# Performance work log

Measured on AMD Instinct MI355X. Metric: run time of the kernel, lower is better.

## Reference

```python
import jax, jax.numpy as jnp
import numpy as np
import math

D_MODEL = 2048
NUM_HEADS = 16
HEAD_DIM = D_MODEL // NUM_HEADS  # 128
B, S = 2, 2048


def setup_inputs() -> dict:
    key = jax.random.key(0)
    ks = jax.random.split(key, 11)
    s_in = 1.0 / math.sqrt(D_MODEL)
    return {
        "query": jax.random.normal(ks[0], (B, S, D_MODEL), dtype=jnp.float32),
        "key": jax.random.normal(ks[1], (B, S, D_MODEL), dtype=jnp.float32),
        "value": jax.random.normal(ks[2], (B, S, D_MODEL), dtype=jnp.float32),
        "Wq": jax.random.normal(ks[3], (D_MODEL, D_MODEL), dtype=jnp.float32) * s_in,
        "bq": jnp.zeros((D_MODEL,), dtype=jnp.float32),
        "Wk": jax.random.normal(ks[4], (D_MODEL, HEAD_DIM), dtype=jnp.float32) * s_in,
        "bk": jnp.zeros((HEAD_DIM,), dtype=jnp.float32),
        "Wv": jax.random.normal(ks[5], (D_MODEL, HEAD_DIM), dtype=jnp.float32) * s_in,
        "bv": jnp.zeros((HEAD_DIM,), dtype=jnp.float32),
        "Wo": jax.random.normal(ks[6], (D_MODEL, D_MODEL), dtype=jnp.float32) * s_in,
        "bo": jnp.zeros((D_MODEL,), dtype=jnp.float32),
    }


def reference(query, key, value, Wq, bq, Wk, bk, Wv, bv, Wo, bo):
    b, s, d_model = query.shape
    h, d = NUM_HEADS, HEAD_DIM
    # Projections: Q has h heads, K/V have a single shared head (MQA)
    Q = (query @ Wq + bq).reshape(b, s, h, d).transpose(0, 2, 1, 3)  # [b,h,s,d]
    K = key @ Wk + bk      # [b,s,d]
    V = value @ Wv + bv    # [b,s,d]
    scale = 1.0 / math.sqrt(d)
    # broadcast single K head over all h query heads
    scores = jnp.einsum('bhqd,bkd->bhqk', Q, K) * scale  # [b,h,s,s]
    weights = jax.nn.softmax(scores, axis=-1)
    attn = jnp.einsum('bhqk,bkd->bhqd', weights, V)      # [b,h,s,d]
    attn = attn.transpose(0, 2, 1, 3).reshape(b, s, d_model)
    return attn @ Wo + bo
```

## Files before the change

### kernel.cpp

```cpp
#include <hip/hip_runtime.h>


typedef unsigned short u16;
typedef __attribute__((ext_vector_type(8))) short bf16x8;
typedef __attribute__((ext_vector_type(4))) short bf16x4;
typedef __attribute__((ext_vector_type(4))) float f32x4;

#define D_MODEL 2048
#define SEQ     2048
#define NH      16
#define HD      128
#define BK      32

__device__ __forceinline__ u16 f2bf(float f){
  union { float f; unsigned u; } v; v.f = f;
  unsigned r = (v.u + 0x7FFFu + ((v.u >> 16) & 1u)) >> 16;
  return (u16)r;
}

#if __has_builtin(__builtin_amdgcn_cvt_pk_bf16_f32)
__device__ __forceinline__ unsigned pack2bf(float a, float b){
  auto v = __builtin_amdgcn_cvt_pk_bf16_f32(a, b);
  unsigned u; __builtin_memcpy(&u, &v, 4); return u;
}
#else
__device__ __forceinline__ unsigned pack2bf(float a, float b){
  return (unsigned)f2bf(a) | ((unsigned)f2bf(b) << 16);
}
#endif

__device__ __forceinline__ void gll16(const void* g, void* l){
  __builtin_amdgcn_global_load_lds(
      (const __attribute__((address_space(1))) void*)g,
      (__attribute__((address_space(3))) void*)l, 16, 0, 0);
}

__global__ __launch_bounds__(256) void convert3_kernel(
    const float4* __restrict__ a, const float4* __restrict__ b, const float4* __restrict__ c,
    ushort4* __restrict__ oa, ushort4* __restrict__ ob, ushort4* __restrict__ oc){
  int i = blockIdx.x*256 + threadIdx.x;
  float4 va = a[i], vb = b[i], vc = c[i];
  ushort4 ra, rb, rc;
  ra.x=f2bf(va.x); ra.y=f2bf(va.y); ra.z=f2bf(va.z); ra.w=f2bf(va.w);
  rb.x=f2bf(vb.x); rb.y=f2bf(vb.y); rb.z=f2bf(vb.z); rb.w=f2bf(vb.w);
  rc.x=f2bf(vc.x); rc.y=f2bf(vc.y); rc.z=f2bf(vc.z); rc.w=f2bf(vc.w);
  oa[i]=ra; ob[i]=rb; oc[i]=rc;
}

__global__ __launch_bounds__(256) void transpose_all(
    const float* __restrict__ Wq, const float* __restrict__ Wo,
    const float* __restrict__ Wk, const float* __restrict__ Wv,
    u16* __restrict__ WqT, u16* __restrict__ WoT,
    u16* __restrict__ WkT, u16* __restrict__ WvT){
  __shared__ float tt[32][33];
  int id = blockIdx.x;
  const float* in; u16* outp; int C, bx, by;
  if (id < 4096)      { in=Wq; outp=WqT; C=2048; bx=id&63;        by=id>>6; }
  else if (id < 8192) { id-=4096; in=Wo; outp=WoT; C=2048; bx=id&63; by=id>>6; }
  else if (id < 8448) { id-=8192; in=Wk; outp=WkT; C=128;  bx=id&3;  by=id>>2; }
  else                { id-=8448; in=Wv; outp=WvT; C=128;  bx=id&3;  by=id>>2; }
  const int R = 2048;
  int c0 = bx*32, r0 = by*32;
  int tx = threadIdx.x & 31, ty = threadIdx.x >> 5;
  #pragma unroll
  for (int k=0;k<4;k++) tt[ty+k*8][tx] = in[(size_t)(r0+ty+k*8)*C + c0+tx];
  __syncthreads();
  #pragma unroll
  for (int k=0;k<4;k++) outp[(size_t)(c0+ty+k*8)*R + r0+tx] = f2bf(tt[tx][ty+k*8]);
}

__device__ __forceinline__ void gemm_core_db(
    const u16* __restrict__ A, const u16* __restrict__ BT,
    int lda, int ldb, int m0, int n0, int kbeg, int kend,
    u16* As, u16* Bs, f32x4 acc[4][4])
{
  const int t = threadIdx.x;
  const int w = t >> 6, l = t & 63;
  const int wr = w >> 1, wc = w & 1;
  const int c16 = l & 15, q = l >> 4;
  const int srow = l >> 2;
  const int sc   = ((l & 3) ^ ((l >> 3) & 3)) * 8;

  int aoff[4], boff[4];
  #pragma unroll
  for (int mt=0;mt<4;mt++){
    int row = wr*64 + mt*16 + c16;
    aoff[mt] = row*BK + ((q ^ ((row>>1)&3))*8);
  }
  #pragma unroll
  for (int nt=0;nt<4;nt++){
    int row = wc*64 + nt*16 + c16;
    boff[nt] = row*BK + ((q ^ ((row>>1)&3))*8);
  }

  auto issue = [&](int k0, int buf){
    u16* Ad = As + buf*4096;
    u16* Bd = Bs + buf*4096;
    #pragma unroll
    for (int half=0; half<2; half++){
      int r = half*64 + w*16 + srow;
      gll16(A  + (size_t)(m0+r)*lda + k0 + sc, Ad + (half*64 + w*16)*BK);
      gll16(BT + (size_t)(n0+r)*ldb + k0 + sc, Bd + (half*64 + w*16)*BK);
    }
  };

  const int n = (kend - kbeg) / BK;
  issue(kbeg, 0);
  for (int i = 0; i < n; i++){
    __syncthreads();
    if (i+1 < n) issue(kbeg + (i+1)*BK, (i+1)&1);
    const u16* Ab = As + (i&1)*4096;
    const u16* Bb = Bs + (i&1)*4096;
    bf16x8 af[4], bfr[4];
    #pragma unroll
    for (int mt=0;mt<4;mt++) af[mt]  = *(const bf16x8*)(Ab + aoff[mt]);
    #pragma unroll
    for (int nt=0;nt<4;nt++) bfr[nt] = *(const bf16x8*)(Bb + boff[nt]);
    #pragma unroll
    for (int mt=0;mt<4;mt++)
      #pragma unroll
      for (int nt=0;nt<4;nt++)
        acc[mt][nt] = __builtin_amdgcn_mfma_f32_16x16x32_bf16(af[mt], bfr[nt], acc[mt][nt], 0,0,0);
  }
}

__global__ __launch_bounds__(256) void proj_kernel(
    const u16* __restrict__ qb, const u16* __restrict__ kb, const u16* __restrict__ vb,
    const u16* __restrict__ WqT, const u16* __restrict__ WkT, const u16* __restrict__ WvT,
    const float* __restrict__ bq, u16* __restrict__ Qp, float* __restrict__ part)
{
  __shared__ u16 As[2*4096], Bs[2*4096];
  f32x4 acc[4][4];
  f32x4 z = {0.f,0.f,0.f,0.f};
  #pragma unroll
  for (int i=0;i<4;i++) for (int j=0;j<4;j++) acc[i][j] = z;
  const int t = threadIdx.x, w = t>>6, l = t&63, wr = w>>1, wc = w&1, c16 = l&15, q = l>>4;
  int id = blockIdx.x;
  if (id < 512){
    int m0 = (id & 31)*128, n0 = (id >> 5)*128;
    gemm_core_db(qb, WqT, 2048, 2048, m0, n0, 0, 2048, As, Bs, acc);
    #pragma unroll
    for (int mt=0;mt<4;mt++)
      #pragma unroll
      for (int nt=0;nt<4;nt++){
        int col = n0 + wc*64 + nt*16 + c16;
        float bv = bq[col];
        #pragma unroll
        for (int r=0;r<4;r++){
          int row = m0 + wr*64 + mt*16 + q*4 + r;
          Qp[(size_t)row*D_MODEL + col] = f2bf(acc[mt][nt][r] + bv);
        }
      }
  } else {
    int kvid = id - 512;
    int zi = kvid & 3, nb = (kvid >> 2) & 1, mi = kvid >> 3;
    const u16* Am = nb ? vb  : kb;
    const u16* Bm = nb ? WvT : WkT;
    gemm_core_db(Am, Bm, 2048, 2048, mi*128, 0, zi*512, zi*512+512, As, Bs, acc);
    float* dst = part + (size_t)(zi*2 + nb)*524288;
    #pragma unroll
    for (int mt=0;mt<4;mt++)
      #pragma unroll
      for (int nt=0;nt<4;nt++){
        int col = wc*64 + nt*16 + c16;
        #pragma unroll
        for (int r=0;r<4;r++){
          int row = mi*128 + wr*64 + mt*16 + q*4 + r;
          dst[(size_t)row*128 + col] = acc[mt][nt][r];
        }
      }
  }
}

__global__ __launch_bounds__(256) void oproj_kernel(
    const u16* __restrict__ A, const u16* __restrict__ BT, const float* __restrict__ bias,
    float* __restrict__ C)
{
  __shared__ u16 As[2*4096], Bs[2*4096];
  f32x4 acc[4][4];
  f32x4 z = {0.f,0.f,0.f,0.f};
  #pragma unroll
  for (int i=0;i<4;i++) for (int j=0;j<4;j++) acc[i][j] = z;
  int m0 = blockIdx.x*128, n0 = blockIdx.y*128;
  gemm_core_db(A, BT, 2048, 2048, m0, n0, 0, 2048, As, Bs, acc);
  const int t = threadIdx.x, w = t>>6, l = t&63, wr = w>>1, wc = w&1, c16 = l&15, q = l>>4;
  #pragma unroll
  for (int mt=0;mt<4;mt++)
    #pragma unroll
    for (int nt=0;nt<4;nt++){
      int col = n0 + wc*64 + nt*16 + c16;
      float bv = bias[col];
      #pragma unroll
      for (int r=0;r<4;r++){
        int row = m0 + wr*64 + mt*16 + q*4 + r;
        C[(size_t)row*D_MODEL + col] = acc[mt][nt][r] + bv;
      }
    }
}

__global__ __launch_bounds__(256) void kv_reduce_kernel(
    const float* __restrict__ part, const float* __restrict__ bk, const float* __restrict__ bv,
    u16* __restrict__ Kp, u16* __restrict__ VpT){
  int idx = blockIdx.x*256 + threadIdx.x;
  int d = idx & 127, sg = idx >> 7;
  float ka = 0.f, va = 0.f;
  #pragma unroll
  for (int zi=0; zi<4; zi++){
    ka += part[(size_t)(zi*2+0)*524288 + idx];
    va += part[(size_t)(zi*2+1)*524288 + idx];
  }
  Kp[idx] = f2bf(ka + bk[d]);
  int b = sg >> 11, sl = sg & 2047;
  VpT[(size_t)b*262144 + (size_t)d*2048 + sl] = f2bf(va + bv[d]);
}

__global__ __launch_bounds__(512, 2) void attn_kernel(
    const u16* __restrict__ Qp, const u16* __restrict__ Kp,
    const u16* __restrict__ VpT, u16* __restrict__ attnb){
  __shared__ u16 lds[32768];
  u16* Ks = lds;
  u16* Vs = lds + 16384;
  const int t = threadIdx.x;
  const int w = t >> 6, l = t & 63;
  const int c16 = l & 15, q = l >> 4;

  const int qt = blockIdx.x;
  const int bh = blockIdx.y;
  const int b = bh >> 4, h = bh & 15;

  const u16* Qbase = Qp  + ((size_t)(b*SEQ + qt*256 + w*32))*D_MODEL + h*HD;
  const u16* Kbase = Kp  + (size_t)(b*SEQ)*HD;
  const u16* Vbase = VpT + (size_t)b*HD*SEQ;

  #pragma unroll
  for (int j=0;j<4;j++){
    int r = j*32 + w*4 + (l >> 4);
    int g = (l & 15) ^ (r & 15);
    gll16(Kbase + (size_t)r*HD + g*8, Ks + j*4096 + w*512);
  }
  bf16x8 qf[2][4];
  #pragma unroll
  for (int qs=0;qs<2;qs++)
    #pragma unroll
    for (int kk=0;kk<4;kk++)
      qf[qs][kk] = *(const bf16x8*)(Qbase + (size_t)(qs*16 + c16)*D_MODEL + (kk*4 + q)*8);
  __syncthreads();

  f32x4 o[2][8];
  f32x4 z4 = {0.f,0.f,0.f,0.f};
  #pragma unroll
  for (int qs=0;qs<2;qs++) for (int dt=0;dt<8;dt++) o[qs][dt] = z4;
  float mrow[2] = {-1e30f, -1e30f};
  float lrow[2] = {0.f, 0.f};
  const float cs = 0.08838834764831845f * 1.4426950408889634f;

  for (int kt = 0; kt < 16; kt++){
    #pragma unroll
    for (int j=0;j<4;j++){
      int d = j*32 + w*4 + (l >> 4);
      int g = (l & 15) ^ (d & 15);
      gll16(Vbase + (size_t)d*SEQ + kt*128 + g*8, Vs + j*4096 + w*512);
    }

    f32x4 s[2][8];
    #pragma unroll
    for (int qs=0;qs<2;qs++) for (int kt8=0;kt8<8;kt8++) s[qs][kt8] = z4;
    __builtin_amdgcn_s_setprio(1);
    #pragma unroll
    for (int kt8=0; kt8<8; kt8++){
      #pragma unroll
      for (int kk=0;kk<4;kk++){
        int ch = kk*4 + q;
        bf16x8 kf = *(const bf16x8*)(Ks + (kt8*16 + c16)*128 + ((ch ^ c16) & 15)*8);
        s[0][kt8] = __builtin_amdgcn_mfma_f32_16x16x32_bf16(kf, qf[0][kk], s[0][kt8], 0,0,0);
        s[1][kt8] = __builtin_amdgcn_mfma_f32_16x16x32_bf16(kf, qf[1][kk], s[1][kt8], 0,0,0);
      }
    }
    __builtin_amdgcn_s_setprio(0);

    float alpha[2];
    #pragma unroll
    for (int qs=0; qs<2; qs++){
      float x[8];
      #pragma unroll
      for (int kt8=0;kt8<8;kt8++)
        x[kt8] = fmaxf(fmaxf(s[qs][kt8][0],s[qs][kt8][1]), fmaxf(s[qs][kt8][2],s[qs][kt8][3]));
      float vmax = fmaxf(fmaxf(fmaxf(x[0],x[1]),fmaxf(x[2],x[3])),
                         fmaxf(fmaxf(x[4],x[5]),fmaxf(x[6],x[7])));
      vmax = fmaxf(vmax, __shfl_xor(vmax, 16));
      vmax = fmaxf(vmax, __shfl_xor(vmax, 32));
      float mnew = fmaxf(mrow[qs], vmax);
      alpha[qs] = exp2f((mrow[qs] - mnew)*cs);
      float mc = mnew*cs;
      float rs[8];
      #pragma unroll
      for (int kt8=0;kt8<8;kt8++){
        float p0 = exp2f(__builtin_fmaf(s[qs][kt8][0], cs, -mc));
        float p1 = exp2f(__builtin_fmaf(s[qs][kt8][1], cs, -mc));
        float p2 = exp2f(__builtin_fmaf(s[qs][kt8][2], cs, -mc));
        float p3 = exp2f(__builtin_fmaf(s[qs][kt8][3], cs, -mc));
        s[qs][kt8][0]=p0; s[qs][kt8][1]=p1; s[qs][kt8][2]=p2; s[qs][kt8][3]=p3;
        rs[kt8] = (p0+p1)+(p2+p3);
      }
      float rsum = ((rs[0]+rs[1])+(rs[2]+rs[3])) + ((rs[4]+rs[5])+(rs[6]+rs[7]));
      rsum += __shfl_xor(rsum, 16);
      rsum += __shfl_xor(rsum, 32);
      lrow[qs] = lrow[qs]*alpha[qs] + rsum;
      mrow[qs] = mnew;
    }

    unsigned long long allone = __ballot(alpha[0] == 1.f && alpha[1] == 1.f);
    if (allone != ~0ull){
      #pragma unroll
      for (int qs=0;qs<2;qs++)
        #pragma unroll
        for (int dt=0;dt<8;dt++)
          #pragma unroll
          for (int r=0;r<4;r++) o[qs][dt][r] *= alpha[qs];
    }

    union PU { unsigned u[4]; bf16x8 v; } P32[2][4];
    #pragma unroll
    for (int qs=0;qs<2;qs++)
      #pragma unroll
      for (int kb=0;kb<4;kb++){
        P32[qs][kb].u[0] = pack2bf(s[qs][2*kb][0],   s[qs][2*kb][1]);
        P32[qs][kb].u[1] = pack2bf(s[qs][2*kb][2],   s[qs][2*kb][3]);
        P32[qs][kb].u[2] = pack2bf(s[qs][2*kb+1][0], s[qs][2*kb+1][1]);
        P32[qs][kb].u[3] = pack2bf(s[qs][2*kb+1][2], s[qs][2*kb+1][3]);
      }

    __syncthreads();

    if (kt < 15){
      #pragma unroll
      for (int j=0;j<4;j++){
        int r = j*32 + w*4 + (l >> 4);
        int g = (l & 15) ^ (r & 15);
        gll16(Kbase + (size_t)((kt+1)*128 + r)*HD + g*8, Ks + j*4096 + w*512);
      }
    }

    __builtin_amdgcn_s_setprio(1);
    #pragma unroll
    for (int kb=0; kb<4; kb++){
      int ca = 4*kb + (q>>1);
      int cb = ca + 2;
      #pragma unroll
      for (int dt=0; dt<8; dt++){
        int d = dt*16 + c16;
        union VU { bf16x4 h[2]; bf16x8 v; } vf;
        vf.h[0] = *(const bf16x4*)(Vs + d*128 + ((ca ^ c16) & 15)*8 + (q&1)*4);
        vf.h[1] = *(const bf16x4*)(Vs + d*128 + ((cb ^ c16) & 15)*8 + (q&1)*4);
        o[0][dt] = __builtin_amdgcn_mfma_f32_16x16x32_bf16(vf.v, P32[0][kb].v, o[0][dt], 0,0,0);
        o[1][dt] = __builtin_amdgcn_mfma_f32_16x16x32_bf16(vf.v, P32[1][kb].v, o[1][dt], 0,0,0);
      }
    }
    __builtin_amdgcn_s_setprio(0);
    __syncthreads();
  }

  #pragma unroll
  for (int qs=0;qs<2;qs++){
    float inv = 1.f / lrow[qs];
    int qrow = qt*256 + w*32 + qs*16 + c16;
    u16* dst = attnb + ((size_t)(b*SEQ) + qrow)*D_MODEL + h*HD + q*4;
    #pragma unroll
    for (int dt=0;dt<8;dt++){
      ushort4 pk;
      pk.x = f2bf(o[qs][dt][0]*inv);
      pk.y = f2bf(o[qs][dt][1]*inv);
      pk.z = f2bf(o[qs][dt][2]*inv);
      pk.w = f2bf(o[qs][dt][3]*inv);
      *(ushort4*)(dst + dt*16) = pk;
    }
  }
}

extern "C" void kernel_launch(void* const* d_in, const int* in_sizes, int n_in,
                              void* d_out, int out_size, void* d_ws, size_t ws_size,
                              hipStream_t stream) {
  (void)in_sizes; (void)n_in; (void)out_size; (void)ws_size;
  const float* query = (const float*)d_in[0];
  const float* key   = (const float*)d_in[1];
  const float* value = (const float*)d_in[2];
  const float* Wq    = (const float*)d_in[3];
  const float* bq    = (const float*)d_in[4];
  const float* Wk    = (const float*)d_in[5];
  const float* bk    = (const float*)d_in[6];
  const float* Wv    = (const float*)d_in[7];
  const float* bv    = (const float*)d_in[8];
  const float* Wo    = (const float*)d_in[9];
  const float* bo    = (const float*)d_in[10];
  float* out = (float*)d_out;

  char* W = (char*)d_ws;
  u16*  qb     = (u16*) (W + 0);
  u16*  kb     = (u16*) (W + 16777216);
  u16*  vb     = (u16*) (W + 33554432);
  u16*  WqT    = (u16*) (W + 50331648);
  u16*  WoT    = (u16*) (W + 58720256);
  u16*  WkT    = (u16*) (W + 67108864);
  u16*  WvT    = (u16*) (W + 67633152);
  u16*  Qp     = (u16*) (W + 68157440);
  u16*  Kp     = (u16*) (W + 84934656);
  u16*  VpT    = (u16*) (W + 85983232);
  u16*  attnb  = (u16*) (W + 87031808);
  float* kvpart= (float*)(W + 103809024);

  convert3_kernel<<<8192, 256, 0, stream>>>(
      (const float4*)query, (const float4*)key, (const float4*)value,
      (ushort4*)qb, (ushort4*)kb, (ushort4*)vb);
  transpose_all<<<8704, 256, 0, stream>>>(Wq, Wo, Wk, Wv, WqT, WoT, WkT, WvT);
  proj_kernel<<<768, 256, 0, stream>>>(qb, kb, vb, WqT, WkT, WvT, bq, Qp, kvpart);
  kv_reduce_kernel<<<2048, 256, 0, stream>>>(kvpart, bk, bv, Kp, VpT);
  attn_kernel<<<dim3(8,32), 512, 0, stream>>>(Qp, Kp, VpT, attnb);
  oproj_kernel<<<dim3(32,16), 256, 0, stream>>>(attnb, WoT, bo, out);
}
```

Measured before the change: 410.6 us.

## Double-buffer K/V tiles in attention with smaller blocks and lazy rescaling

```diff
diff --git a/kernel.cpp b/kernel.cpp
--- a/kernel.cpp
+++ b/kernel.cpp
@@ -214,12 +214,10 @@
   VpT[(size_t)b*262144 + (size_t)d*2048 + sl] = f2bf(va + bv[d]);
 }
 
-__global__ __launch_bounds__(512, 2) void attn_kernel(
+__global__ __launch_bounds__(256, 2) void attn_kernel(
     const u16* __restrict__ Qp, const u16* __restrict__ Kp,
     const u16* __restrict__ VpT, u16* __restrict__ attnb){
   __shared__ u16 lds[32768];
-  u16* Ks = lds;
-  u16* Vs = lds + 16384;
   const int t = threadIdx.x;
   const int w = t >> 6, l = t & 63;
   const int c16 = l & 15, q = l >> 4;
@@ -228,15 +226,24 @@
   const int bh = blockIdx.y;
   const int b = bh >> 4, h = bh & 15;
 
-  const u16* Qbase = Qp  + ((size_t)(b*SEQ + qt*256 + w*32))*D_MODEL + h*HD;
+  const u16* Qbase = Qp  + ((size_t)(b*SEQ + qt*128 + w*32))*D_MODEL + h*HD;
   const u16* Kbase = Kp  + (size_t)(b*SEQ)*HD;
   const u16* Vbase = VpT + (size_t)b*HD*SEQ;
 
+  const int kr  = w*4 + (l >> 4);
+  const int kpc = l & 15;
+  const int vd0 = w*8 + (l >> 3);
+  const int vpc = l & 7;
+
   #pragma unroll
   for (int j=0;j<4;j++){
-    int r = j*32 + w*4 + (l >> 4);
-    int g = (l & 15) ^ (r & 15);
-    gll16(Kbase + (size_t)r*HD + g*8, Ks + j*4096 + w*512);
+    int r = j*16 + kr;
+    gll16(Kbase + (size_t)r*HD + ((kpc ^ (r & 15))*8), lds + j*2048 + w*512);
+  }
+  #pragma unroll
+  for (int j=0;j<4;j++){
+    int d = j*32 + vd0;
+    gll16(Vbase + (size_t)d*SEQ + ((vpc ^ (d & 7))*8), lds + 16384 + j*2048 + w*512);
   }
   bf16x8 qf[2][4];
   #pragma unroll
@@ -254,22 +261,36 @@
   float lrow[2] = {0.f, 0.f};
   const float cs = 0.08838834764831845f * 1.4426950408889634f;
 
-  for (int kt = 0; kt < 16; kt++){
-    #pragma unroll
-    for (int j=0;j<4;j++){
-      int d = j*32 + w*4 + (l >> 4);
-      int g = (l & 15) ^ (d & 15);
-      gll16(Vbase + (size_t)d*SEQ + kt*128 + g*8, Vs + j*4096 + w*512);
-    }
-
-    f32x4 s[2][8];
-    #pragma unroll
-    for (int qs=0;qs<2;qs++) for (int kt8=0;kt8<8;kt8++) s[qs][kt8] = z4;
+  for (int kt = 0; kt < 32; kt++){
+    const int p = kt & 1;
+    if (kt < 31){
+      u16* Kd = lds + (p^1)*8192;
+      u16* Vd = lds + 16384 + (p^1)*8192;
+      #pragma unroll
+      for (int j=0;j<4;j++){
+        int r = j*16 + kr;
+        gll16(Kbase + (size_t)((kt+1)*64 + r)*HD + ((kpc ^ (r & 15))*8), Kd + j*2048 + w*512);
+      }
+      #pragma unroll
+      for (int j=0;j<4;j++){
+        int d = j*32 + vd0;
+        gll16(Vbase + (size_t)d*SEQ + (kt+1)*64 + ((vpc ^ (d & 7))*8), Vd + j*2048 + w*512);
+      }
+    }
+    const u16* Ks = lds + p*8192;
+    const u16* Vs = lds + 16384 + p*8192;
+
+    f32x4 s[2][4];
     __builtin_amdgcn_s_setprio(1);
     #pragma unroll
-    for (int kt8=0; kt8<8; kt8++){
-      #pragma unroll
-      for (int kk=0;kk<4;kk++){
+    for (int kt8=0; kt8<4; kt8++){
+      {
+        bf16x8 kf = *(const bf16x8*)(Ks + (kt8*16 + c16)*128 + ((q ^ c16) & 15)*8);
+        s[0][kt8] = __builtin_amdgcn_mfma_f32_16x16x32_bf16(kf, qf[0][0], z4, 0,0,0);
+        s[1][kt8] = __builtin_amdgcn_mfma_f32_16x16x32_bf16(kf, qf[1][0], z4, 0,0,0);
+      }
+      #pragma unroll
+      for (int kk=1;kk<4;kk++){
         int ch = kk*4 + q;
         bf16x8 kf = *(const bf16x8*)(Ks + (kt8*16 + c16)*128 + ((ch ^ c16) & 15)*8);
         s[0][kt8] = __builtin_amdgcn_mfma_f32_16x16x32_bf16(kf, qf[0][kk], s[0][kt8], 0,0,0);
@@ -278,80 +299,69 @@
     }
     __builtin_amdgcn_s_setprio(0);
 
-    float alpha[2];
+    float vmax[2];
     #pragma unroll
     for (int qs=0; qs<2; qs++){
-      float x[8];
-      #pragma unroll
-      for (int kt8=0;kt8<8;kt8++)
-        x[kt8] = fmaxf(fmaxf(s[qs][kt8][0],s[qs][kt8][1]), fmaxf(s[qs][kt8][2],s[qs][kt8][3]));
-      float vmax = fmaxf(fmaxf(fmaxf(x[0],x[1]),fmaxf(x[2],x[3])),
-                         fmaxf(fmaxf(x[4],x[5]),fmaxf(x[6],x[7])));
-      vmax = fmaxf(vmax, __shfl_xor(vmax, 16));
-      vmax = fmaxf(vmax, __shfl_xor(vmax, 32));
-      float mnew = fmaxf(mrow[qs], vmax);
-      alpha[qs] = exp2f((mrow[qs] - mnew)*cs);
-      float mc = mnew*cs;
-      float rs[8];
-      #pragma unroll
-      for (int kt8=0;kt8<8;kt8++){
+      float x0 = fmaxf(fmaxf(s[qs][0][0],s[qs][0][1]), fmaxf(s[qs][0][2],s[qs][0][3]));
+      float x1 = fmaxf(fmaxf(s[qs][1][0],s[qs][1][1]), fmaxf(s[qs][1][2],s[qs][1][3]));
+      float x2 = fmaxf(fmaxf(s[qs][2][0],s[qs][2][1]), fmaxf(s[qs][2][2],s[qs][2][3]));
+      float x3 = fmaxf(fmaxf(s[qs][3][0],s[qs][3][1]), fmaxf(s[qs][3][2],s[qs][3][3]));
+      float vm = fmaxf(fmaxf(x0,x1), fmaxf(x2,x3));
+      vm = fmaxf(vm, __shfl_xor(vm, 16));
+      vm = fmaxf(vm, __shfl_xor(vm, 32));
+      vmax[qs] = vm;
+    }
+    bool upd = ((vmax[0]-mrow[0])*cs > 8.f) || ((vmax[1]-mrow[1])*cs > 8.f);
+    if (__any(upd)){
+      #pragma unroll
+      for (int qs=0; qs<2; qs++){
+        float mnew = fmaxf(mrow[qs], vmax[qs]);
+        float a = exp2f((mrow[qs]-mnew)*cs);
+        mrow[qs] = mnew; lrow[qs] *= a;
+        #pragma unroll
+        for (int dt=0;dt<8;dt++)
+          #pragma unroll
+          for (int r=0;r<4;r++) o[qs][dt][r] *= a;
+      }
+    }
+    union PU { unsigned u[4]; bf16x8 v; } P32[2][2];
+    #pragma unroll
+    for (int qs=0; qs<2; qs++){
+      float mc = mrow[qs]*cs;
+      float rsum = 0.f;
+      #pragma unroll
+      for (int kt8=0;kt8<4;kt8++){
         float p0 = exp2f(__builtin_fmaf(s[qs][kt8][0], cs, -mc));
         float p1 = exp2f(__builtin_fmaf(s[qs][kt8][1], cs, -mc));
         float p2 = exp2f(__builtin_fmaf(s[qs][kt8][2], cs, -mc));
         float p3 = exp2f(__builtin_fmaf(s[qs][kt8][3], cs, -mc));
         s[qs][kt8][0]=p0; s[qs][kt8][1]=p1; s[qs][kt8][2]=p2; s[qs][kt8][3]=p3;
-        rs[kt8] = (p0+p1)+(p2+p3);
-      }
-      float rsum = ((rs[0]+rs[1])+(rs[2]+rs[3])) + ((rs[4]+rs[5])+(rs[6]+rs[7]));
+        rsum += (p0+p1)+(p2+p3);
+      }
       rsum += __shfl_xor(rsum, 16);
       rsum += __shfl_xor(rsum, 32);
-      lrow[qs] = lrow[qs]*alpha[qs] + rsum;
-      mrow[qs] = mnew;
-    }
-
-    unsigned long long allone = __ballot(alpha[0] == 1.f && alpha[1] == 1.f);
-    if (allone != ~0ull){
-      #pragma unroll
-      for (int qs=0;qs<2;qs++)
-        #pragma unroll
-        for (int dt=0;dt<8;dt++)
-          #pragma unroll
-          for (int r=0;r<4;r++) o[qs][dt][r] *= alpha[qs];
-    }
-
-    union PU { unsigned u[4]; bf16x8 v; } P32[2][4];
-    #pragma unroll
-    for (int qs=0;qs<2;qs++)
-      #pragma unroll
-      for (int kb=0;kb<4;kb++){
-        P32[qs][kb].u[0] = pack2bf(s[qs][2*kb][0],   s[qs][2*kb][1]);
-        P32[qs][kb].u[1] = pack2bf(s[qs][2*kb][2],   s[qs][2*kb][3]);
-        P32[qs][kb].u[2] = pack2bf(s[qs][2*kb+1][0], s[qs][2*kb+1][1]);
-        P32[qs][kb].u[3] = pack2bf(s[qs][2*kb+1][2], s[qs][2*kb+1][3]);
-      }
-
-    __syncthreads();
-
-    if (kt < 15){
-      #pragma unroll
-      for (int j=0;j<4;j++){
-        int r = j*32 + w*4 + (l >> 4);
-        int g = (l & 15) ^ (r & 15);
-        gll16(Kbase + (size_t)((kt+1)*128 + r)*HD + g*8, Ks + j*4096 + w*512);
-      }
+      lrow[qs] += rsum;
+      P32[qs][0].u[0] = pack2bf(s[qs][0][0], s[qs][0][1]);
+      P32[qs][0].u[1] = pack2bf(s[qs][0][2], s[qs][0][3]);
+      P32[qs][0].u[2] = pack2bf(s[qs][1][0], s[qs][1][1]);
+      P32[qs][0].u[3] = pack2bf(s[qs][1][2], s[qs][1][3]);
+      P32[qs][1].u[0] = pack2bf(s[qs][2][0], s[qs][2][1]);
+      P32[qs][1].u[1] = pack2bf(s[qs][2][2], s[qs][2][3]);
+      P32[qs][1].u[2] = pack2bf(s[qs][3][0], s[qs][3][1]);
+      P32[qs][1].u[3] = pack2bf(s[qs][3][2], s[qs][3][3]);
     }
 
     __builtin_amdgcn_s_setprio(1);
     #pragma unroll
-    for (int kb=0; kb<4; kb++){
+    for (int kb=0; kb<2; kb++){
       int ca = 4*kb + (q>>1);
       int cb = ca + 2;
       #pragma unroll
       for (int dt=0; dt<8; dt++){
         int d = dt*16 + c16;
-        union VU { bf16x4 h[2]; bf16x8 v; } vf;
-        vf.h[0] = *(const bf16x4*)(Vs + d*128 + ((ca ^ c16) & 15)*8 + (q&1)*4);
-        vf.h[1] = *(const bf16x4*)(Vs + d*128 + ((cb ^ c16) & 15)*8 + (q&1)*4);
+        union VU { bf16x4 hh[2]; bf16x8 v; } vf;
+        vf.hh[0] = *(const bf16x4*)(Vs + d*64 + ((ca ^ (d&7)) & 7)*8 + (q&1)*4);
+        vf.hh[1] = *(const bf16x4*)(Vs + d*64 + ((cb ^ (d&7)) & 7)*8 + (q&1)*4);
         o[0][dt] = __builtin_amdgcn_mfma_f32_16x16x32_bf16(vf.v, P32[0][kb].v, o[0][dt], 0,0,0);
         o[1][dt] = __builtin_amdgcn_mfma_f32_16x16x32_bf16(vf.v, P32[1][kb].v, o[1][dt], 0,0,0);
       }
@@ -363,7 +373,7 @@
   #pragma unroll
   for (int qs=0;qs<2;qs++){
     float inv = 1.f / lrow[qs];
-    int qrow = qt*256 + w*32 + qs*16 + c16;
+    int qrow = qt*128 + w*32 + qs*16 + c16;
     u16* dst = attnb + ((size_t)(b*SEQ) + qrow)*D_MODEL + h*HD + q*4;
     #pragma unroll
     for (int dt=0;dt<8;dt++){
@@ -414,6 +424,6 @@
   transpose_all<<<8704, 256, 0, stream>>>(Wq, Wo, Wk, Wv, WqT, WoT, WkT, WvT);
   proj_kernel<<<768, 256, 0, stream>>>(qb, kb, vb, WqT, WkT, WvT, bq, Qp, kvpart);
   kv_reduce_kernel<<<2048, 256, 0, stream>>>(kvpart, bk, bv, Kp, VpT);
-  attn_kernel<<<dim3(8,32), 512, 0, stream>>>(Qp, Kp, VpT, attnb);
+  attn_kernel<<<dim3(16,32), 256, 0, stream>>>(Qp, Kp, VpT, attnb);
   oproj_kernel<<<dim3(32,16), 256, 0, stream>>>(attnb, WoT, bo, out);
 }
```

New measurement: 412.8 us. Within noise of the previous version (+0.5%).
